# Kernel tuning notes

Measured on AMD Instinct MI355X. Metric: run time of the kernel, lower is better.

The kernel has to match this reference:

```python
import jax, jax.numpy as jnp
import numpy as np

B, T, I, H, O = 256, 100, 1024, 2048, 10

def setup_inputs() -> dict:
    key = jax.random.key(0)
    k = jax.random.split(key, 6)
    return {
        "x": jax.random.normal(k[0], (B, T, I), dtype=jnp.float32),
        "h0": jax.random.normal(k[1], (B, H), dtype=jnp.float32),
        "Win": jax.random.uniform(k[2], (I, H), dtype=jnp.float32, minval=-0.1, maxval=0.1),
        "W": jax.random.normal(k[3], (H, H), dtype=jnp.float32) * 0.01,
        "lin_w": jax.random.normal(k[4], (O, H), dtype=jnp.float32) * 0.02,
        "lin_b": jax.random.normal(k[5], (O,), dtype=jnp.float32) * 0.02,
    }

def reference(x, h0, Win, W, lin_w, lin_b):
    xin = jnp.einsum('bti,ih->bth', x, Win)  # precompute input projection for all steps

    def step(h, xin_t):
        h = jnp.tanh(xin_t + h @ W)
        y = h @ lin_w.T + lin_b
        return h, y

    _, ys = jax.lax.scan(step, h0, jnp.swapaxes(xin, 0, 1))  # ys: [T, B, O]
    return jnp.swapaxes(ys, 0, 1)  # [B, T, O]
```

## Files before the change

kernel.cpp:

```cpp
#include <hip/hip_runtime.h>
#include <math.h>

#define Bn 256
#define Tn 100
#define In 1024
#define Hn 2048
#define On 10
#define Kc (In + Hn)

typedef short s8v  __attribute__((ext_vector_type(8)));
typedef unsigned short us4 __attribute__((ext_vector_type(4)));
typedef float f32x4 __attribute__((ext_vector_type(4)));

__device__ __forceinline__ unsigned short f2bf(float f) {
    unsigned int u = __float_as_uint(f);
    u += 0x7fffu + ((u >> 16) & 1u);
    return (unsigned short)(u >> 16);
}

__device__ __forceinline__ float fast_tanh(float x) {
    float e = __expf(x + x);
    return 1.0f - 2.0f * __builtin_amdgcn_rcpf(e + 1.0f);
}


__global__ void conv_x_kernel(const float4* __restrict__ src, ushort4* __restrict__ dst) {
    int i = blockIdx.x * 256 + threadIdx.x;
    float4 v = src[i];
    ushort4 o;
    o.x = f2bf(v.x); o.y = f2bf(v.y); o.z = f2bf(v.z); o.w = f2bf(v.w);
    dst[i] = o;
}

__global__ void transpose_bf16_kernel(const float* __restrict__ src, unsigned short* __restrict__ dst,
                                      int N, int ld, int colOff) {
    __shared__ float tile[32][33];
    int k0 = blockIdx.x * 32;
    int n0 = blockIdx.y * 32;
    int c = threadIdx.x & 31;
    int r = threadIdx.x >> 5;
    #pragma unroll
    for (int i = 0; i < 32; i += 8)
        tile[r + i][c] = src[(size_t)(k0 + r + i) * N + n0 + c];
    __syncthreads();
    #pragma unroll
    for (int i = 0; i < 32; i += 8)
        dst[(size_t)(n0 + r + i) * ld + colOff + k0 + c] = f2bf(tile[c][r + i]);
}

__global__ void small_conv_kernel(const float* __restrict__ h0, const float* __restrict__ lin_w,
                                  unsigned short* __restrict__ h_all0, unsigned short* __restrict__ lwb,
                                  unsigned int* __restrict__ bar) {
    int idx = blockIdx.x * 256 + threadIdx.x;
    if (idx < 512) bar[idx] = 0u;
    if (idx < Bn * Hn) {
        h_all0[idx] = f2bf(h0[idx]);
    } else {
        int j = idx - Bn * Hn;
        int o = j >> 11;
        int k = j & 2047;
        lwb[j] = (o < On) ? f2bf(lin_w[o * Hn + k]) : (unsigned short)0;
    }
}

__global__ __launch_bounds__(512, 2)
void scan_kernel(const unsigned short* __restrict__ xb,
                 const unsigned short* __restrict__ BTm,
                 unsigned short* __restrict__ h_all,
                 unsigned int* __restrict__ bar) {
    const int g = blockIdx.x;
    const int mg = (g >> 3) & 3;
    const int m0 = mg * 64;
    const int n0 = ((g & 7) * 8 + (g >> 5)) * 32;
    const int w = threadIdx.x >> 6;
    const int lane = threadIdx.x & 63;
    const int quad = lane >> 4;
    const int lr = lane & 15;

    __shared__ float red[8][64][36];

    const unsigned short* bp0 = BTm + (size_t)(n0 + lr) * Kc;
    const unsigned short* bp1 = BTm + (size_t)(n0 + 16 + lr) * Kc;

    const size_t xrow = (size_t)Tn * In;

    const int fidx = mg * 64 + (g & 7) * 8 + (g >> 5);
    unsigned int* fl = bar + mg * 64;

    s8v bx[4][2];
    s8v bh[8][2];
    #pragma unroll
    for (int c = 0; c < 4; ++c) {
        const int kq = w * 128 + c * 32 + quad * 8;
        bx[c][0] = *(const s8v*)(bp0 + kq);
        bx[c][1] = *(const s8v*)(bp1 + kq);
    }
    #pragma unroll
    for (int c = 0; c < 8; ++c) {
        const int kq = In + w * 256 + c * 32 + quad * 8;
        bh[c][0] = *(const s8v*)(bp0 + kq);
        bh[c][1] = *(const s8v*)(bp1 + kq);
    }

    f32x4 acc[4][2];
    #pragma unroll
    for (int mi = 0; mi < 4; ++mi)
        #pragma unroll
        for (int ni = 0; ni < 2; ++ni)
            acc[mi][ni] = (f32x4){0.f, 0.f, 0.f, 0.f};

    {
        const unsigned short* xt = xb + 0 * In;
        #pragma unroll
        for (int c = 0; c < 4; ++c) {
            const int kq = w * 128 + c * 32 + quad * 8;
            const unsigned short* arow = xt + kq + (size_t)(m0 + lr) * xrow;
            s8v a0 = *(const s8v*)(arow);
            s8v a1 = *(const s8v*)(arow + 16 * xrow);
            s8v a2 = *(const s8v*)(arow + 32 * xrow);
            s8v a3 = *(const s8v*)(arow + 48 * xrow);
            acc[0][0] = __builtin_amdgcn_mfma_f32_16x16x32_bf16(a0, bx[c][0], acc[0][0], 0, 0, 0);
            acc[1][0] = __builtin_amdgcn_mfma_f32_16x16x32_bf16(a1, bx[c][0], acc[1][0], 0, 0, 0);
            acc[2][0] = __builtin_amdgcn_mfma_f32_16x16x32_bf16(a2, bx[c][0], acc[2][0], 0, 0, 0);
            acc[3][0] = __builtin_amdgcn_mfma_f32_16x16x32_bf16(a3, bx[c][0], acc[3][0], 0, 0, 0);
            acc[0][1] = __builtin_amdgcn_mfma_f32_16x16x32_bf16(a0, bx[c][1], acc[0][1], 0, 0, 0);
            acc[1][1] = __builtin_amdgcn_mfma_f32_16x16x32_bf16(a1, bx[c][1], acc[1][1], 0, 0, 0);
            acc[2][1] = __builtin_amdgcn_mfma_f32_16x16x32_bf16(a2, bx[c][1], acc[2][1], 0, 0, 0);
            acc[3][1] = __builtin_amdgcn_mfma_f32_16x16x32_bf16(a3, bx[c][1], acc[3][1], 0, 0, 0);
        }
    }

    for (int t = 0; t < Tn; ++t) {
        const unsigned short* hrow = h_all + (size_t)t * (Bn * Hn)
                                   + (size_t)(m0 + lr) * Hn + w * 256 + quad * 8;
        s8v A[2][4];
        #pragma unroll
        for (int r = 0; r < 4; ++r)
            A[0][r] = *(const s8v*)(hrow + r * 16 * Hn);
        #pragma unroll
        for (int c = 0; c < 8; ++c) {
            if (c < 7) {
                const unsigned short* p = hrow + (c + 1) * 32;
                #pragma unroll
                for (int r = 0; r < 4; ++r)
                    A[(c + 1) & 1][r] = *(const s8v*)(p + r * 16 * Hn);
            }
            const s8v a0 = A[c & 1][0];
            const s8v a1 = A[c & 1][1];
            const s8v a2 = A[c & 1][2];
            const s8v a3 = A[c & 1][3];
            acc[0][0] = __builtin_amdgcn_mfma_f32_16x16x32_bf16(a0, bh[c][0], acc[0][0], 0, 0, 0);
            acc[1][0] = __builtin_amdgcn_mfma_f32_16x16x32_bf16(a1, bh[c][0], acc[1][0], 0, 0, 0);
            acc[2][0] = __builtin_amdgcn_mfma_f32_16x16x32_bf16(a2, bh[c][0], acc[2][0], 0, 0, 0);
            acc[3][0] = __builtin_amdgcn_mfma_f32_16x16x32_bf16(a3, bh[c][0], acc[3][0], 0, 0, 0);
            acc[0][1] = __builtin_amdgcn_mfma_f32_16x16x32_bf16(a0, bh[c][1], acc[0][1], 0, 0, 0);
            acc[1][1] = __builtin_amdgcn_mfma_f32_16x16x32_bf16(a1, bh[c][1], acc[1][1], 0, 0, 0);
            acc[2][1] = __builtin_amdgcn_mfma_f32_16x16x32_bf16(a2, bh[c][1], acc[2][1], 0, 0, 0);
            acc[3][1] = __builtin_amdgcn_mfma_f32_16x16x32_bf16(a3, bh[c][1], acc[3][1], 0, 0, 0);
        }

        #pragma unroll
        for (int mi = 0; mi < 4; ++mi)
            #pragma unroll
            for (int ni = 0; ni < 2; ++ni)
                #pragma unroll
                for (int rr = 0; rr < 4; ++rr)
                    red[w][mi * 16 + quad * 4 + rr][ni * 16 + lr] = acc[mi][ni][rr];
        __syncthreads();

        {
            int j = threadIdx.x << 2;
            int row = j >> 5;
            int c0 = j & 31;
            float4 s0 = *(const float4*)&red[0][row][c0];
            float4 s1 = *(const float4*)&red[1][row][c0];
            float4 s2 = *(const float4*)&red[2][row][c0];
            float4 s3 = *(const float4*)&red[3][row][c0];
            float4 s4 = *(const float4*)&red[4][row][c0];
            float4 s5 = *(const float4*)&red[5][row][c0];
            float4 s6 = *(const float4*)&red[6][row][c0];
            float4 s7 = *(const float4*)&red[7][row][c0];
            us4 o4;
            o4[0] = f2bf(fast_tanh(((s0.x + s1.x) + (s2.x + s3.x)) + ((s4.x + s5.x) + (s6.x + s7.x))));
            o4[1] = f2bf(fast_tanh(((s0.y + s1.y) + (s2.y + s3.y)) + ((s4.y + s5.y) + (s6.y + s7.y))));
            o4[2] = f2bf(fast_tanh(((s0.z + s1.z) + (s2.z + s3.z)) + ((s4.z + s5.z) + (s6.z + s7.z))));
            o4[3] = f2bf(fast_tanh(((s0.w + s1.w) + (s2.w + s3.w)) + ((s4.w + s5.w) + (s6.w + s7.w))));
            unsigned long long* dst = (unsigned long long*)
                (h_all + (size_t)(t + 1) * (Bn * Hn) + (size_t)(m0 + row) * Hn + n0 + c0);
            __hip_atomic_store(dst, __builtin_bit_cast(unsigned long long, o4),
                               __ATOMIC_RELAXED, __HIP_MEMORY_SCOPE_AGENT);
        }

        if (t < Tn - 1) {
            __syncthreads();
            const unsigned int tp1 = (unsigned int)(t + 1);

            if (threadIdx.x == 0)
                __hip_atomic_store(bar + fidx, tp1, __ATOMIC_RELAXED,
                                   __HIP_MEMORY_SCOPE_AGENT);

            #pragma unroll
            for (int mi = 0; mi < 4; ++mi)
                #pragma unroll
                for (int ni = 0; ni < 2; ++ni)
                    acc[mi][ni] = (f32x4){0.f, 0.f, 0.f, 0.f};
            const unsigned short* xt = xb + (size_t)(t + 1) * In;
            #pragma unroll
            for (int c = 0; c < 4; ++c) {
                const int kq = w * 128 + c * 32 + quad * 8;
                const unsigned short* arow = xt + kq + (size_t)(m0 + lr) * xrow;
                s8v a0 = *(const s8v*)(arow);
                s8v a1 = *(const s8v*)(arow + 16 * xrow);
                s8v a2 = *(const s8v*)(arow + 32 * xrow);
                s8v a3 = *(const s8v*)(arow + 48 * xrow);
                acc[0][0] = __builtin_amdgcn_mfma_f32_16x16x32_bf16(a0, bx[c][0], acc[0][0], 0, 0, 0);
                acc[1][0] = __builtin_amdgcn_mfma_f32_16x16x32_bf16(a1, bx[c][0], acc[1][0], 0, 0, 0);
                acc[2][0] = __builtin_amdgcn_mfma_f32_16x16x32_bf16(a2, bx[c][0], acc[2][0], 0, 0, 0);
                acc[3][0] = __builtin_amdgcn_mfma_f32_16x16x32_bf16(a3, bx[c][0], acc[3][0], 0, 0, 0);
                acc[0][1] = __builtin_amdgcn_mfma_f32_16x16x32_bf16(a0, bx[c][1], acc[0][1], 0, 0, 0);
                acc[1][1] = __builtin_amdgcn_mfma_f32_16x16x32_bf16(a1, bx[c][1], acc[1][1], 0, 0, 0);
                acc[2][1] = __builtin_amdgcn_mfma_f32_16x16x32_bf16(a2, bx[c][1], acc[2][1], 0, 0, 0);
                acc[3][1] = __builtin_amdgcn_mfma_f32_16x16x32_bf16(a3, bx[c][1], acc[3][1], 0, 0, 0);
            }

            while (true) {
                unsigned int v = __hip_atomic_load(fl + lane, __ATOMIC_RELAXED,
                                                   __HIP_MEMORY_SCOPE_AGENT);
                if (__all((int)(v >= tp1))) break;
                __builtin_amdgcn_s_sleep(1);
            }
            asm volatile("" ::: "memory");
        }
    }
}

__global__ __launch_bounds__(256)
void gemm2_kernel(const unsigned short* __restrict__ h_all, const unsigned short* __restrict__ lwb,
                  const float* __restrict__ lb, float* __restrict__ y) {
    int gw = blockIdx.x * 4 + (threadIdx.x >> 6);
    int lane = threadIdx.x & 63, quad = lane >> 4, lr = lane & 15;
    int m0 = gw * 16;
    int t = m0 >> 8;
    int b0 = m0 & 255;
    const unsigned short* ah = h_all + ((size_t)(t + 1) * Bn + b0 + lr) * Hn + quad * 8;
    const unsigned short* bh = lwb + (size_t)lr * Hn + quad * 8;
    f32x4 acc0 = {0.f, 0.f, 0.f, 0.f}, acc1 = {0.f, 0.f, 0.f, 0.f};
    #pragma unroll
    for (int k0 = 0; k0 < Hn; k0 += 64) {
        s8v a0 = *(const s8v*)(ah + k0);
        s8v b0 = *(const s8v*)(bh + k0);
        acc0 = __builtin_amdgcn_mfma_f32_16x16x32_bf16(a0, b0, acc0, 0, 0, 0);
        s8v a1 = *(const s8v*)(ah + k0 + 32);
        s8v b1 = *(const s8v*)(bh + k0 + 32);
        acc1 = __builtin_amdgcn_mfma_f32_16x16x32_bf16(a1, b1, acc1, 0, 0, 0);
    }
    acc0 = acc0 + acc1;
    if (lr < On) {
        float bias = lb[lr];
        #pragma unroll
        for (int rr = 0; rr < 4; ++rr) {
            int b = b0 + quad * 4 + rr;
            y[(size_t)b * (Tn * On) + t * On + lr] = acc0[rr] + bias;
        }
    }
}


extern "C" void kernel_launch(void* const* d_in, const int* in_sizes, int n_in,
                              void* d_out, int out_size, void* d_ws, size_t ws_size,
                              hipStream_t stream) {
    const float* x   = (const float*)d_in[0];
    const float* h0  = (const float*)d_in[1];
    const float* Win = (const float*)d_in[2];
    const float* W   = (const float*)d_in[3];
    const float* lw  = (const float*)d_in[4];
    const float* lb  = (const float*)d_in[5];
    float* y = (float*)d_out;

    unsigned short* ws    = (unsigned short*)d_ws;
    unsigned short* xb    = ws;
    unsigned short* BTm   = xb + (size_t)Bn * Tn * In;
    unsigned short* h_all = BTm + (size_t)Hn * Kc;
    unsigned short* lwb   = h_all + (size_t)(Tn + 1) * Bn * Hn;
    unsigned int*   bar   = (unsigned int*)(lwb + 32768);

    conv_x_kernel<<<25600, 256, 0, stream>>>((const float4*)x, (ushort4*)xb);
    transpose_bf16_kernel<<<dim3(32, 64), 256, 0, stream>>>(Win, BTm, Hn, Kc, 0);
    transpose_bf16_kernel<<<dim3(64, 64), 256, 0, stream>>>(W, BTm, Hn, Kc, In);
    small_conv_kernel<<<2176, 256, 0, stream>>>(h0, lw, h_all, lwb, bar);

    scan_kernel<<<256, 512, 0, stream>>>(xb, BTm, h_all, bar);

    gemm2_kernel<<<400, 256, 0, stream>>>(h_all, lwb, lb, y);
}
```

Measured before the change: 1.375 ms.

## Halve scan workgroup to 4 waves with doubled K-slice per wave

The persistent scan kernel now runs 4 waves of 256 threads instead of 8, so each wave owns twice as much of the K dimension. It holds twice as many weight fragments in registers and issues all h-row and x-row loads up front rather than double-buffering them. The cross-wave LDS reduction shrinks to 4 partials, and each thread reduces and stores 8 outputs. The aim is to cut reduction and barrier cost and raise memory-level parallelism per step, at the cost of much higher register pressure (possible spills) and fewer waves to hide latency.

Result: slower. 1.630 ms (+18.5%).

```diff
diff --git a/kernel.cpp b/kernel.cpp
--- a/kernel.cpp
+++ b/kernel.cpp
@@ -63,7 +63,7 @@
     }
 }
 
-__global__ __launch_bounds__(512, 2)
+__global__ __launch_bounds__(256, 1)
 void scan_kernel(const unsigned short* __restrict__ xb,
                  const unsigned short* __restrict__ BTm,
                  unsigned short* __restrict__ h_all,
@@ -77,7 +77,7 @@
     const int quad = lane >> 4;
     const int lr = lane & 15;
 
-    __shared__ float red[8][64][36];
+    __shared__ float red[4][64][36];
 
     const unsigned short* bp0 = BTm + (size_t)(n0 + lr) * Kc;
     const unsigned short* bp1 = BTm + (size_t)(n0 + 16 + lr) * Kc;
@@ -87,17 +87,17 @@
     const int fidx = mg * 64 + (g & 7) * 8 + (g >> 5);
     unsigned int* fl = bar + mg * 64;
 
-    s8v bx[4][2];
-    s8v bh[8][2];
-    #pragma unroll
-    for (int c = 0; c < 4; ++c) {
-        const int kq = w * 128 + c * 32 + quad * 8;
+    s8v bx[8][2];
+    s8v bh[16][2];
+    #pragma unroll
+    for (int c = 0; c < 8; ++c) {
+        const int kq = w * 256 + c * 32 + quad * 8;
         bx[c][0] = *(const s8v*)(bp0 + kq);
         bx[c][1] = *(const s8v*)(bp1 + kq);
     }
     #pragma unroll
-    for (int c = 0; c < 8; ++c) {
-        const int kq = In + w * 256 + c * 32 + quad * 8;
+    for (int c = 0; c < 16; ++c) {
+        const int kq = In + w * 512 + c * 32 + quad * 8;
         bh[c][0] = *(const s8v*)(bp0 + kq);
         bh[c][1] = *(const s8v*)(bp1 + kq);
     }
@@ -110,53 +110,50 @@
             acc[mi][ni] = (f32x4){0.f, 0.f, 0.f, 0.f};
 
     {
-        const unsigned short* xt = xb + 0 * In;
-        #pragma unroll
-        for (int c = 0; c < 4; ++c) {
-            const int kq = w * 128 + c * 32 + quad * 8;
-            const unsigned short* arow = xt + kq + (size_t)(m0 + lr) * xrow;
-            s8v a0 = *(const s8v*)(arow);
-            s8v a1 = *(const s8v*)(arow + 16 * xrow);
-            s8v a2 = *(const s8v*)(arow + 32 * xrow);
-            s8v a3 = *(const s8v*)(arow + 48 * xrow);
-            acc[0][0] = __builtin_amdgcn_mfma_f32_16x16x32_bf16(a0, bx[c][0], acc[0][0], 0, 0, 0);
-            acc[1][0] = __builtin_amdgcn_mfma_f32_16x16x32_bf16(a1, bx[c][0], acc[1][0], 0, 0, 0);
-            acc[2][0] = __builtin_amdgcn_mfma_f32_16x16x32_bf16(a2, bx[c][0], acc[2][0], 0, 0, 0);
-            acc[3][0] = __builtin_amdgcn_mfma_f32_16x16x32_bf16(a3, bx[c][0], acc[3][0], 0, 0, 0);
-            acc[0][1] = __builtin_amdgcn_mfma_f32_16x16x32_bf16(a0, bx[c][1], acc[0][1], 0, 0, 0);
-            acc[1][1] = __builtin_amdgcn_mfma_f32_16x16x32_bf16(a1, bx[c][1], acc[1][1], 0, 0, 0);
-            acc[2][1] = __builtin_amdgcn_mfma_f32_16x16x32_bf16(a2, bx[c][1], acc[2][1], 0, 0, 0);
-            acc[3][1] = __builtin_amdgcn_mfma_f32_16x16x32_bf16(a3, bx[c][1], acc[3][1], 0, 0, 0);
+        const unsigned short* ar = xb + w * 256 + quad * 8 + (size_t)(m0 + lr) * xrow;
+        s8v X[8][4];
+        #pragma unroll
+        for (int c = 0; c < 8; ++c)
+            #pragma unroll
+            for (int r = 0; r < 4; ++r)
+                X[c][r] = *(const s8v*)(ar + c * 32 + r * 16 * xrow);
+        #pragma unroll
+        for (int c = 0; c < 8; ++c) {
+            acc[0][0] = __builtin_amdgcn_mfma_f32_16x16x32_bf16(X[c][0], bx[c][0], acc[0][0], 0, 0, 0);
+            acc[1][0] = __builtin_amdgcn_mfma_f32_16x16x32_bf16(X[c][1], bx[c][0], acc[1][0], 0, 0, 0);
+            acc[2][0] = __builtin_amdgcn_mfma_f32_16x16x32_bf16(X[c][2], bx[c][0], acc[2][0], 0, 0, 0);
+            acc[3][0] = __builtin_amdgcn_mfma_f32_16x16x32_bf16(X[c][3], bx[c][0], acc[3][0], 0, 0, 0);
+            acc[0][1] = __builtin_amdgcn_mfma_f32_16x16x32_bf16(X[c][0], bx[c][1], acc[0][1], 0, 0, 0);
+            acc[1][1] = __builtin_amdgcn_mfma_f32_16x16x32_bf16(X[c][1], bx[c][1], acc[1][1], 0, 0, 0);
+            acc[2][1] = __builtin_amdgcn_mfma_f32_16x16x32_bf16(X[c][2], bx[c][1], acc[2][1], 0, 0, 0);
+            acc[3][1] = __builtin_amdgcn_mfma_f32_16x16x32_bf16(X[c][3], bx[c][1], acc[3][1], 0, 0, 0);
         }
     }
 
     for (int t = 0; t < Tn; ++t) {
-        const unsigned short* hrow = h_all + (size_t)t * (Bn * Hn)
-                                   + (size_t)(m0 + lr) * Hn + w * 256 + quad * 8;
-        s8v A[2][4];
-        #pragma unroll
-        for (int r = 0; r < 4; ++r)
-            A[0][r] = *(const s8v*)(hrow + r * 16 * Hn);
-        #pragma unroll
-        for (int c = 0; c < 8; ++c) {
-            if (c < 7) {
-                const unsigned short* p = hrow + (c + 1) * 32;
+        const unsigned short* hr = h_all + (size_t)t * (Bn * Hn)
+                                 + (size_t)(m0 + lr) * Hn + w * 512 + quad * 8;
+        s8v A[16][4];
+        #pragma unroll
+        for (int c = 0; c < 8; ++c)
+            #pragma unroll
+            for (int r = 0; r < 4; ++r)
+                A[c][r] = *(const s8v*)(hr + c * 32 + r * 16 * Hn);
+        #pragma unroll
+        for (int c = 0; c < 16; ++c) {
+            if (c < 8) {
                 #pragma unroll
                 for (int r = 0; r < 4; ++r)
-                    A[(c + 1) & 1][r] = *(const s8v*)(p + r * 16 * Hn);
+                    A[c + 8][r] = *(const s8v*)(hr + (c + 8) * 32 + r * 16 * Hn);
             }
-            const s8v a0 = A[c & 1][0];
-            const s8v a1 = A[c & 1][1];
-            const s8v a2 = A[c & 1][2];
-            const s8v a3 = A[c & 1][3];
-            acc[0][0] = __builtin_amdgcn_mfma_f32_16x16x32_bf16(a0, bh[c][0], acc[0][0], 0, 0, 0);
-            acc[1][0] = __builtin_amdgcn_mfma_f32_16x16x32_bf16(a1, bh[c][0], acc[1][0], 0, 0, 0);
-            acc[2][0] = __builtin_amdgcn_mfma_f32_16x16x32_bf16(a2, bh[c][0], acc[2][0], 0, 0, 0);
-            acc[3][0] = __builtin_amdgcn_mfma_f32_16x16x32_bf16(a3, bh[c][0], acc[3][0], 0, 0, 0);
-            acc[0][1] = __builtin_amdgcn_mfma_f32_16x16x32_bf16(a0, bh[c][1], acc[0][1], 0, 0, 0);
-            acc[1][1] = __builtin_amdgcn_mfma_f32_16x16x32_bf16(a1, bh[c][1], acc[1][1], 0, 0, 0);
-            acc[2][1] = __builtin_amdgcn_mfma_f32_16x16x32_bf16(a2, bh[c][1], acc[2][1], 0, 0, 0);
-            acc[3][1] = __builtin_amdgcn_mfma_f32_16x16x32_bf16(a3, bh[c][1], acc[3][1], 0, 0, 0);
+            acc[0][0] = __builtin_amdgcn_mfma_f32_16x16x32_bf16(A[c][0], bh[c][0], acc[0][0], 0, 0, 0);
+            acc[1][0] = __builtin_amdgcn_mfma_f32_16x16x32_bf16(A[c][1], bh[c][0], acc[1][0], 0, 0, 0);
+            acc[2][0] = __builtin_amdgcn_mfma_f32_16x16x32_bf16(A[c][2], bh[c][0], acc[2][0], 0, 0, 0);
+            acc[3][0] = __builtin_amdgcn_mfma_f32_16x16x32_bf16(A[c][3], bh[c][0], acc[3][0], 0, 0, 0);
+            acc[0][1] = __builtin_amdgcn_mfma_f32_16x16x32_bf16(A[c][0], bh[c][1], acc[0][1], 0, 0, 0);
+            acc[1][1] = __builtin_amdgcn_mfma_f32_16x16x32_bf16(A[c][1], bh[c][1], acc[1][1], 0, 0, 0);
+            acc[2][1] = __builtin_amdgcn_mfma_f32_16x16x32_bf16(A[c][2], bh[c][1], acc[2][1], 0, 0, 0);
+            acc[3][1] = __builtin_amdgcn_mfma_f32_16x16x32_bf16(A[c][3], bh[c][1], acc[3][1], 0, 0, 0);
         }
 
         #pragma unroll
@@ -169,25 +166,31 @@
         __syncthreads();
 
         {
-            int j = threadIdx.x << 2;
+            int j = threadIdx.x << 3;
             int row = j >> 5;
             int c0 = j & 31;
-            float4 s0 = *(const float4*)&red[0][row][c0];
-            float4 s1 = *(const float4*)&red[1][row][c0];
-            float4 s2 = *(const float4*)&red[2][row][c0];
-            float4 s3 = *(const float4*)&red[3][row][c0];
-            float4 s4 = *(const float4*)&red[4][row][c0];
-            float4 s5 = *(const float4*)&red[5][row][c0];
-            float4 s6 = *(const float4*)&red[6][row][c0];
-            float4 s7 = *(const float4*)&red[7][row][c0];
-            us4 o4;
-            o4[0] = f2bf(fast_tanh(((s0.x + s1.x) + (s2.x + s3.x)) + ((s4.x + s5.x) + (s6.x + s7.x))));
-            o4[1] = f2bf(fast_tanh(((s0.y + s1.y) + (s2.y + s3.y)) + ((s4.y + s5.y) + (s6.y + s7.y))));
-            o4[2] = f2bf(fast_tanh(((s0.z + s1.z) + (s2.z + s3.z)) + ((s4.z + s5.z) + (s6.z + s7.z))));
-            o4[3] = f2bf(fast_tanh(((s0.w + s1.w) + (s2.w + s3.w)) + ((s4.w + s5.w) + (s6.w + s7.w))));
+            float4 a0 = *(const float4*)&red[0][row][c0];
+            float4 a1 = *(const float4*)&red[1][row][c0];
+            float4 a2 = *(const float4*)&red[2][row][c0];
+            float4 a3 = *(const float4*)&red[3][row][c0];
+            float4 b0 = *(const float4*)&red[0][row][c0 + 4];
+            float4 b1 = *(const float4*)&red[1][row][c0 + 4];
+            float4 b2 = *(const float4*)&red[2][row][c0 + 4];
+            float4 b3 = *(const float4*)&red[3][row][c0 + 4];
+            us4 oA, oB;
+            oA[0] = f2bf(fast_tanh((a0.x + a1.x) + (a2.x + a3.x)));
+            oA[1] = f2bf(fast_tanh((a0.y + a1.y) + (a2.y + a3.y)));
+            oA[2] = f2bf(fast_tanh((a0.z + a1.z) + (a2.z + a3.z)));
+            oA[3] = f2bf(fast_tanh((a0.w + a1.w) + (a2.w + a3.w)));
+            oB[0] = f2bf(fast_tanh((b0.x + b1.x) + (b2.x + b3.x)));
+            oB[1] = f2bf(fast_tanh((b0.y + b1.y) + (b2.y + b3.y)));
+            oB[2] = f2bf(fast_tanh((b0.z + b1.z) + (b2.z + b3.z)));
+            oB[3] = f2bf(fast_tanh((b0.w + b1.w) + (b2.w + b3.w)));
             unsigned long long* dst = (unsigned long long*)
                 (h_all + (size_t)(t + 1) * (Bn * Hn) + (size_t)(m0 + row) * Hn + n0 + c0);
-            __hip_atomic_store(dst, __builtin_bit_cast(unsigned long long, o4),
+            __hip_atomic_store(dst, __builtin_bit_cast(unsigned long long, oA),
+                               __ATOMIC_RELAXED, __HIP_MEMORY_SCOPE_AGENT);
+            __hip_atomic_store(dst + 1, __builtin_bit_cast(unsigned long long, oB),
                                __ATOMIC_RELAXED, __HIP_MEMORY_SCOPE_AGENT);
         }
 
@@ -204,23 +207,24 @@
                 #pragma unroll
                 for (int ni = 0; ni < 2; ++ni)
                     acc[mi][ni] = (f32x4){0.f, 0.f, 0.f, 0.f};
-            const unsigned short* xt = xb + (size_t)(t + 1) * In;
-            #pragma unroll
-            for (int c = 0; c < 4; ++c) {
-                const int kq = w * 128 + c * 32 + quad * 8;
-                const unsigned short* arow = xt + kq + (size_t)(m0 + lr) * xrow;
-                s8v a0 = *(const s8v*)(arow);
-                s8v a1 = *(const s8v*)(arow + 16 * xrow);
-                s8v a2 = *(const s8v*)(arow + 32 * xrow);
-                s8v a3 = *(const s8v*)(arow + 48 * xrow);
-                acc[0][0] = __builtin_amdgcn_mfma_f32_16x16x32_bf16(a0, bx[c][0], acc[0][0], 0, 0, 0);
-                acc[1][0] = __builtin_amdgcn_mfma_f32_16x16x32_bf16(a1, bx[c][0], acc[1][0], 0, 0, 0);
-                acc[2][0] = __builtin_amdgcn_mfma_f32_16x16x32_bf16(a2, bx[c][0], acc[2][0], 0, 0, 0);
-                acc[3][0] = __builtin_amdgcn_mfma_f32_16x16x32_bf16(a3, bx[c][0], acc[3][0], 0, 0, 0);
-                acc[0][1] = __builtin_amdgcn_mfma_f32_16x16x32_bf16(a0, bx[c][1], acc[0][1], 0, 0, 0);
-                acc[1][1] = __builtin_amdgcn_mfma_f32_16x16x32_bf16(a1, bx[c][1], acc[1][1], 0, 0, 0);
-                acc[2][1] = __builtin_amdgcn_mfma_f32_16x16x32_bf16(a2, bx[c][1], acc[2][1], 0, 0, 0);
-                acc[3][1] = __builtin_amdgcn_mfma_f32_16x16x32_bf16(a3, bx[c][1], acc[3][1], 0, 0, 0);
+            const unsigned short* ar = xb + (size_t)(t + 1) * In + w * 256 + quad * 8
+                                     + (size_t)(m0 + lr) * xrow;
+            s8v X[8][4];
+            #pragma unroll
+            for (int c = 0; c < 8; ++c)
+                #pragma unroll
+                for (int r = 0; r < 4; ++r)
+                    X[c][r] = *(const s8v*)(ar + c * 32 + r * 16 * xrow);
+            #pragma unroll
+            for (int c = 0; c < 8; ++c) {
+                acc[0][0] = __builtin_amdgcn_mfma_f32_16x16x32_bf16(X[c][0], bx[c][0], acc[0][0], 0, 0, 0);
+                acc[1][0] = __builtin_amdgcn_mfma_f32_16x16x32_bf16(X[c][1], bx[c][0], acc[1][0], 0, 0, 0);
+                acc[2][0] = __builtin_amdgcn_mfma_f32_16x16x32_bf16(X[c][2], bx[c][0], acc[2][0], 0, 0, 0);
+                acc[3][0] = __builtin_amdgcn_mfma_f32_16x16x32_bf16(X[c][3], bx[c][0], acc[3][0], 0, 0, 0);
+                acc[0][1] = __builtin_amdgcn_mfma_f32_16x16x32_bf16(X[c][0], bx[c][1], acc[0][1], 0, 0, 0);
+                acc[1][1] = __builtin_amdgcn_mfma_f32_16x16x32_bf16(X[c][1], bx[c][1], acc[1][1], 0, 0, 0);
+                acc[2][1] = __builtin_amdgcn_mfma_f32_16x16x32_bf16(X[c][2], bx[c][1], acc[2][1], 0, 0, 0);
+                acc[3][1] = __builtin_amdgcn_mfma_f32_16x16x32_bf16(X[c][3], bx[c][1], acc[3][1], 0, 0, 0);
             }
 
             while (true) {
@@ -289,7 +293,7 @@
     transpose_bf16_kernel<<<dim3(64, 64), 256, 0, stream>>>(W, BTm, Hn, Kc, In);
     small_conv_kernel<<<2176, 256, 0, stream>>>(h0, lw, h_all, lwb, bar);
 
-    scan_kernel<<<256, 512, 0, stream>>>(xb, BTm, h_all, bar);
+    scan_kernel<<<256, 256, 0, stream>>>(xb, BTm, h_all, bar);
 
     gemm2_kernel<<<400, 256, 0, stream>>>(h_all, lwb, lb, y);
 }
```
